# Performance work log

Hardware: AMD Instinct MI355X
Metric: run time of the kernel (lower is better)

The kernel has to match this reference:

```python
import jax, jax.numpy as jnp
import numpy as np

TEMPERATURE = 1.0

def setup_inputs() -> dict:
    key = jax.random.key(0)
    k1, k2 = jax.random.split(key)
    B, F, C = 16384, 2048, 1000
    features = jax.random.normal(k1, (B, F), dtype=jnp.float32)
    prototypes = jax.random.normal(k2, (C, F), dtype=jnp.float32)
    return {"features": features, "prototypes": prototypes}

def reference(features, prototypes):
    # Euclidean pairwise distance via ||a||^2 + ||b||^2 - 2 a.b (same math as cdist p=2)
    f_sq = jnp.sum(features * features, axis=-1, keepdims=True)        # [B,1]
    p_sq = jnp.sum(prototypes * prototypes, axis=-1)[None, :]          # [1,C]
    cross = jnp.einsum('bf,cf->bc', features, prototypes)              # [B,C]
    d2 = jnp.maximum(f_sq + p_sq - 2.0 * cross, 0.0)
    distances = jnp.sqrt(d2)
    logits = -distances
    return logits / TEMPERATURE
```

## Files before the change

kernel.cpp:

```cpp
#include <hip/hip_runtime.h>
#include <stdint.h>


#define KDIM 2048

typedef __attribute__((ext_vector_type(8))) __bf16 bf16x8;
typedef __attribute__((ext_vector_type(4))) float f32x4;

__device__ __forceinline__ bool sniff_is_f32(const void* Araw) {
  const uint16_t* sniff = (const uint16_t*)Araw;
  float mx = 0.f;
#pragma unroll
  for (int i = 0; i < 64; ++i) {
    float v = __uint_as_float(((uint32_t)sniff[i]) << 16);
    mx = fmaxf(mx, fabsf(v));
  }
  return mx > 1e4f;
}

__device__ __forceinline__ uint32_t bf16rn(uint32_t u) {
  return (u + 0x7FFFu + ((u >> 16) & 1u)) >> 16;
}
__device__ __forceinline__ uint32_t pack_rn(uint32_t a, uint32_t b) {
  return bf16rn(a) | (bf16rn(b) << 16);
}

__device__ __forceinline__ void gload_lds16(const void* g, void* l) {
  __builtin_amdgcn_global_load_lds(
      (const __attribute__((address_space(1))) void*)g,
      (__attribute__((address_space(3))) void*)l, 16, 0, 0);
}

__global__ __launch_bounds__(256) void prep_kernel(
    const void* __restrict__ Araw, const void* __restrict__ Braw,
    uint16_t* __restrict__ Abf, uint16_t* __restrict__ Bbf,
    float* __restrict__ fsq, float* __restrict__ psq, int M, int N) {
  const bool isf32 = sniff_is_f32(Araw);
  const int wave = threadIdx.x >> 6;
  const int lane = threadIdx.x & 63;
  const int row = blockIdx.x * 4 + wave;
  if (row >= M + N) return;
  const bool isA = row < M;
  const size_t r = isA ? (size_t)row : (size_t)(row - M);
  uint2* dst = (uint2*)((isA ? Abf : Bbf) + r * KDIM);
  float s = 0.f;
  if (isf32) {
    const float* p = (isA ? (const float*)Araw : (const float*)Braw) + r * KDIM;
#pragma unroll
    for (int it = 0; it < KDIM / 256; ++it) {
      float4 v = *((const float4*)p + it * 64 + lane);
      s = fmaf(v.x, v.x, fmaf(v.y, v.y, fmaf(v.z, v.z, fmaf(v.w, v.w, s))));
      uint2 o;
      o.x = pack_rn(__float_as_uint(v.x), __float_as_uint(v.y));
      o.y = pack_rn(__float_as_uint(v.z), __float_as_uint(v.w));
      dst[it * 64 + lane] = o;
    }
  } else {
    const uint16_t* p =
        (isA ? (const uint16_t*)Araw : (const uint16_t*)Braw) + r * KDIM;
#pragma unroll
    for (int it = 0; it < KDIM / 256; ++it) {
      uint2 v = *((const uint2*)p + it * 64 + lane);
      float e0 = __uint_as_float(v.x << 16);
      float e1 = __uint_as_float(v.x & 0xFFFF0000u);
      float e2 = __uint_as_float(v.y << 16);
      float e3 = __uint_as_float(v.y & 0xFFFF0000u);
      s = fmaf(e0, e0, fmaf(e1, e1, fmaf(e2, e2, fmaf(e3, e3, s))));
      dst[it * 64 + lane] = v;
    }
  }
#pragma unroll
  for (int o = 32; o > 0; o >>= 1) s += __shfl_down(s, o, 64);
  if (lane == 0) {
    if (isA) fsq[r] = s;
    else     psq[r] = s;
  }
}

#define BM2 256
#define BN2 256
#define BK2 64
#define NK2 (KDIM / BK2)

__global__ __launch_bounds__(512, 2) void gemm_kernel(
    const uint16_t* __restrict__ Abf, const uint16_t* __restrict__ Bbf,
    const float* __restrict__ fsq, const float* __restrict__ psq,
    float* __restrict__ out, int M, int N) {
  __shared__ uint32_t Ab[2][BM2][32];
  __shared__ uint32_t Bb[2][BN2][32];

  const int tid = threadIdx.x;
  const int lane = tid & 63;
  const int wave = tid >> 6;

  const int gx = gridDim.x, gy = gridDim.y;
  const int nwg = gx * gy;
  int id = blockIdx.y * gx + blockIdx.x;
  if ((nwg & 7) == 0) id = (id & 7) * (nwg >> 3) + (id >> 3);
  const int m0 = (id / gx) * BM2;
  const int n0 = (id % gx) * BN2;

  const int wr = wave >> 2;
  const int wc = wave & 3;
  const int lr = lane & 15;
  const int lg = lane >> 4;

  const int wbase = (tid & ~63);

  auto stage = [&](int b, int ks) {
#pragma unroll
    for (int p = 0; p < 4; ++p) {
      const int f = p * 512 + tid;
      const int row = f >> 3;
      const int gc = (f & 7) ^ (row & 7);
      uint32_t* la = &Ab[b][0][0] + (p * 512 + wbase) * 4;
      uint32_t* lb = &Bb[b][0][0] + (p * 512 + wbase) * 4;
      int gm = m0 + row; gm = gm < M ? gm : M - 1;
      int gn = n0 + row; gn = gn < N ? gn : N - 1;
      gload_lds16(Abf + (size_t)gm * KDIM + ks * BK2 + gc * 8, la);
      gload_lds16(Bbf + (size_t)gn * KDIM + ks * BK2 + gc * 8, lb);
    }
  };

  f32x4 acc[8][4] = {};

  stage(0, 0);

  for (int ks = 0; ks < NK2; ++ks) {
    const int buf = ks & 1;
    if (ks + 1 < NK2) {
      stage(buf ^ 1, ks + 1);
      asm volatile("s_waitcnt vmcnt(8)");
    } else {
      asm volatile("s_waitcnt vmcnt(0)");
    }
    __builtin_amdgcn_s_barrier();
    asm volatile("" ::: "memory");

    bf16x8 bh[4][2];
#pragma unroll
    for (int nj = 0; nj < 4; ++nj) {
      const int r = wc * 64 + nj * 16 + lr;
#pragma unroll
      for (int kk = 0; kk < 2; ++kk) {
        const int pc = ((kk * 4 + lg) ^ (r & 7)) * 4;
        bh[nj][kk] = *(const bf16x8*)&Bb[buf][r][pc];
      }
    }

    __builtin_amdgcn_s_setprio(1);
#pragma unroll
    for (int mi = 0; mi < 8; ++mi) {
      const int r = wr * 128 + mi * 16 + lr;
      const int p0 = ((0 + lg) ^ (r & 7)) * 4;
      const int p1 = ((4 + lg) ^ (r & 7)) * 4;
      const bf16x8 a0 = *(const bf16x8*)&Ab[buf][r][p0];
      const bf16x8 a1 = *(const bf16x8*)&Ab[buf][r][p1];
#pragma unroll
      for (int nj = 0; nj < 4; ++nj) {
        acc[mi][nj] = __builtin_amdgcn_mfma_f32_16x16x32_bf16(
            a0, bh[nj][0], acc[mi][nj], 0, 0, 0);
        acc[mi][nj] = __builtin_amdgcn_mfma_f32_16x16x32_bf16(
            a1, bh[nj][1], acc[mi][nj], 0, 0, 0);
      }
    }
    __builtin_amdgcn_s_setprio(0);

    __builtin_amdgcn_s_barrier();
    asm volatile("" ::: "memory");
  }

#pragma unroll
  for (int nj = 0; nj < 4; ++nj) {
    const int n = n0 + wc * 64 + nj * 16 + lr;
    if (n >= N) continue;
    const float pn = psq[n];
#pragma unroll
    for (int mi = 0; mi < 8; ++mi) {
      const int mb = m0 + wr * 128 + mi * 16 + lg * 4;
#pragma unroll
      for (int r = 0; r < 4; ++r) {
        const int m = mb + r;
        if (m < M) {
          const float d2 = fsq[m] + pn - 2.f * acc[mi][nj][r];
          out[(size_t)m * N + n] = -sqrtf(fmaxf(d2, 0.f));
        }
      }
    }
  }
}

#define BM 128
#define BN 128
#define BKS 32
#define NSTEPS (KDIM / BKS)

__global__ __launch_bounds__(256) void dist_mfma_kernel(
    const void* __restrict__ Araw, const void* __restrict__ Braw,
    float* __restrict__ out, int M, int N) {
  __shared__ uint32_t Ah[2][BM][16];
  __shared__ uint32_t Bh[2][BN][16];
  __shared__ float fsqs[BM];
  __shared__ float psqs[BN];

  const bool isf32 = sniff_is_f32(Araw);
  const int tid = threadIdx.x;
  const int lane = tid & 63;
  const int wave = tid >> 6;
  const int m0 = blockIdx.y * BM;
  const int n0 = blockIdx.x * BN;

  const float* A32 = (const float*)Araw;
  const float* B32 = (const float*)Braw;
  const uint16_t* A16 = (const uint16_t*)Araw;
  const uint16_t* B16 = (const uint16_t*)Braw;

  const int crow = tid >> 2;
  const int cch = tid & 3;
  const int wr = wave >> 1;
  const int wc = wave & 1;
  const int lr = lane & 15;
  const int lg = lane >> 4;

  uint4 qa0[2], qa1[2], qb0[2], qb1[2];
  float na[2] = {0.f, 0.f};
  float nb[2] = {0.f, 0.f};

  auto load_step = [&](int ks) {
#pragma unroll
    for (int s = 0; s < 2; ++s) {
      const int row = crow + 64 * s;
      int gm = m0 + row; gm = gm < M ? gm : M - 1;
      int gn = n0 + row; gn = gn < N ? gn : N - 1;
      const size_t ea = (size_t)gm * KDIM + ks * BKS + cch * 8;
      const size_t eb = (size_t)gn * KDIM + ks * BKS + cch * 8;
      if (isf32) {
        qa0[s] = *(const uint4*)(A32 + ea);
        qa1[s] = *(const uint4*)(A32 + ea + 4);
        qb0[s] = *(const uint4*)(B32 + eb);
        qb1[s] = *(const uint4*)(B32 + eb + 4);
      } else {
        qa0[s] = *(const uint4*)(A16 + ea);
        qb0[s] = *(const uint4*)(B16 + eb);
      }
    }
  };

  auto store_step = [&](int b) {
#pragma unroll
    for (int s = 0; s < 2; ++s) {
      const int row = crow + 64 * s;
      const int pc = (cch ^ ((row >> 1) & 3)) * 4;
      if (isf32) {
        const uint32_t ua[8] = {qa0[s].x, qa0[s].y, qa0[s].z, qa0[s].w,
                                qa1[s].x, qa1[s].y, qa1[s].z, qa1[s].w};
        const uint32_t ub[8] = {qb0[s].x, qb0[s].y, qb0[s].z, qb0[s].w,
                                qb1[s].x, qb1[s].y, qb1[s].z, qb1[s].w};
        float sa = 0.f, sb = 0.f;
#pragma unroll
        for (int j = 0; j < 8; ++j) {
          const float fa = __uint_as_float(ua[j]);
          const float fb = __uint_as_float(ub[j]);
          sa = fmaf(fa, fa, sa);
          sb = fmaf(fb, fb, sb);
        }
        na[s] += sa; nb[s] += sb;
        uint4 pa = {pack_rn(ua[0], ua[1]), pack_rn(ua[2], ua[3]),
                    pack_rn(ua[4], ua[5]), pack_rn(ua[6], ua[7])};
        uint4 pb = {pack_rn(ub[0], ub[1]), pack_rn(ub[2], ub[3]),
                    pack_rn(ub[4], ub[5]), pack_rn(ub[6], ub[7])};
        *(uint4*)&Ah[b][row][pc] = pa;
        *(uint4*)&Bh[b][row][pc] = pb;
      } else {
        float sa = 0.f, sb = 0.f;
        const uint32_t va[4] = {qa0[s].x, qa0[s].y, qa0[s].z, qa0[s].w};
        const uint32_t vb[4] = {qb0[s].x, qb0[s].y, qb0[s].z, qb0[s].w};
#pragma unroll
        for (int j = 0; j < 4; ++j) {
          const float a0 = __uint_as_float(va[j] << 16);
          const float a1 = __uint_as_float(va[j] & 0xFFFF0000u);
          const float b0 = __uint_as_float(vb[j] << 16);
          const float b1 = __uint_as_float(vb[j] & 0xFFFF0000u);
          sa = fmaf(a0, a0, fmaf(a1, a1, sa));
          sb = fmaf(b0, b0, fmaf(b1, b1, sb));
        }
        na[s] += sa; nb[s] += sb;
        *(uint4*)&Ah[b][row][pc] = qa0[s];
        *(uint4*)&Bh[b][row][pc] = qb0[s];
      }
    }
  };

  f32x4 acc[4][4] = {};
  load_step(0);
  store_step(0);
  __syncthreads();

  for (int ks = 0; ks < NSTEPS; ++ks) {
    const int buf = ks & 1;
    const int nxt = ks + 1;
    if (nxt < NSTEPS) load_step(nxt);

    bf16x8 ah[4], bh[4];
#pragma unroll
    for (int i = 0; i < 4; ++i) {
      const int r = wr * 64 + i * 16 + lr;
      const int pc = (lg ^ ((r >> 1) & 3)) * 4;
      ah[i] = *(const bf16x8*)&Ah[buf][r][pc];
    }
#pragma unroll
    for (int j = 0; j < 4; ++j) {
      const int r = wc * 64 + j * 16 + lr;
      const int pc = (lg ^ ((r >> 1) & 3)) * 4;
      bh[j] = *(const bf16x8*)&Bh[buf][r][pc];
    }

#pragma unroll
    for (int i = 0; i < 4; ++i)
#pragma unroll
      for (int j = 0; j < 4; ++j)
        acc[i][j] = __builtin_amdgcn_mfma_f32_16x16x32_bf16(ah[i], bh[j],
                                                            acc[i][j], 0, 0, 0);

    if (nxt < NSTEPS) store_step(nxt & 1);
    __syncthreads();
  }

  float v0 = na[0], v1 = na[1], w0 = nb[0], w1 = nb[1];
#pragma unroll
  for (int o = 1; o <= 2; o <<= 1) {
    v0 += __shfl_xor(v0, o);
    v1 += __shfl_xor(v1, o);
    w0 += __shfl_xor(w0, o);
    w1 += __shfl_xor(w1, o);
  }
  if (cch == 0) {
    fsqs[crow] = v0;
    fsqs[crow + 64] = v1;
    psqs[crow] = w0;
    psqs[crow + 64] = w1;
  }
  __syncthreads();

#pragma unroll
  for (int j = 0; j < 4; ++j) {
    const int nn = wc * 64 + j * 16 + lr;
    const int n = n0 + nn;
    if (n >= N) continue;
    const float pn = psqs[nn];
#pragma unroll
    for (int i = 0; i < 4; ++i) {
      const int mb = wr * 64 + i * 16 + lg * 4;
#pragma unroll
      for (int r = 0; r < 4; ++r) {
        const int m = m0 + mb + r;
        if (m < M) {
          const float d2 = fsqs[mb + r] + pn - 2.f * acc[i][j][r];
          out[(size_t)m * N + n] = -sqrtf(fmaxf(d2, 0.f));
        }
      }
    }
  }
}

extern "C" void kernel_launch(void* const* d_in, const int* in_sizes, int n_in,
                              void* d_out, int out_size, void* d_ws,
                              size_t ws_size, hipStream_t stream) {
  (void)n_in; (void)out_size;
  const void* feat = d_in[0];
  const void* prot = d_in[1];
  float* out = (float*)d_out;

  const int M = in_sizes[0] / KDIM;
  const int N = in_sizes[1] / KDIM;

  const size_t bfA = (size_t)M * KDIM * sizeof(uint16_t);
  const size_t bfB = (size_t)N * KDIM * sizeof(uint16_t);
  const size_t ws_need = bfA + bfB + (size_t)(M + N) * sizeof(float);

  if (d_ws != nullptr && ws_size >= ws_need) {
    uint16_t* Abf = (uint16_t*)d_ws;
    uint16_t* Bbf = (uint16_t*)((char*)d_ws + bfA);
    float* fsq = (float*)((char*)d_ws + bfA + bfB);
    float* psq = fsq + M;
    const int rows = M + N;
    prep_kernel<<<dim3((rows + 3) / 4), dim3(256), 0, stream>>>(
        feat, prot, Abf, Bbf, fsq, psq, M, N);
    dim3 grid((N + BN2 - 1) / BN2, (M + BM2 - 1) / BM2);
    gemm_kernel<<<grid, dim3(512), 0, stream>>>(Abf, Bbf, fsq, psq, out, M, N);
  } else {
    dim3 grid((N + BN - 1) / BN, (M + BM - 1) / BM);
    dist_mfma_kernel<<<grid, dim3(256), 0, stream>>>(feat, prot, out, M, N);
  }
}
```

Baseline: 322.0 us.

## Restructure GEMM main loop into four interleaved MFMA clusters with split prefetch

Splits each K-step into four MFMA clusters over half-tiles of A and B, with LDS fragment reads and global-to-LDS prefetch of the next stage spread between clusters and separated by barriers. The aim is to overlap LDS reads and global loads with MFMA work instead of loading all fragments up front, in the style of ping-pong scheduling. It adds many more workgroup barriers per iteration and a full vmcnt(0) wait before the last cluster, which could serialize the loads and stall.

```diff
diff --git a/kernel.cpp b/kernel.cpp
--- a/kernel.cpp
+++ b/kernel.cpp
@@ -6,6 +6,8 @@
 
 typedef __attribute__((ext_vector_type(8))) __bf16 bf16x8;
 typedef __attribute__((ext_vector_type(4))) float f32x4;
+
+#define BAR() do { asm volatile("" ::: "memory"); __builtin_amdgcn_s_barrier(); asm volatile("" ::: "memory"); } while (0)
 
 __device__ __forceinline__ bool sniff_is_f32(const void* Araw) {
   const uint16_t* sniff = (const uint16_t*)Araw;
@@ -107,67 +109,100 @@
 
   const int wbase = (tid & ~63);
 
-  auto stage = [&](int b, int ks) {
-#pragma unroll
-    for (int p = 0; p < 4; ++p) {
-      const int f = p * 512 + tid;
-      const int row = f >> 3;
+  auto stage_half = [&](int b, int ks, int mat, int h) {
+#pragma unroll
+    for (int l = 0; l < 2; ++l) {
+      const int f = l * 512 + tid;
+      const int row = h * 128 + (f >> 3);
       const int gc = (f & 7) ^ (row & 7);
-      uint32_t* la = &Ab[b][0][0] + (p * 512 + wbase) * 4;
-      uint32_t* lb = &Bb[b][0][0] + (p * 512 + wbase) * 4;
-      int gm = m0 + row; gm = gm < M ? gm : M - 1;
-      int gn = n0 + row; gn = gn < N ? gn : N - 1;
-      gload_lds16(Abf + (size_t)gm * KDIM + ks * BK2 + gc * 8, la);
-      gload_lds16(Bbf + (size_t)gn * KDIM + ks * BK2 + gc * 8, lb);
+      uint32_t* base = mat ? &Bb[b][0][0] : &Ab[b][0][0];
+      uint32_t* dst = base + h * 4096 + (l * 512 + wbase) * 4;
+      const int lim = mat ? N : M;
+      int g = (mat ? n0 : m0) + row;
+      g = g < lim ? g : lim - 1;
+      const uint16_t* G = mat ? Bbf : Abf;
+      gload_lds16(G + (size_t)g * KDIM + ks * BK2 + gc * 8, dst);
+    }
+  };
+
+  bf16x8 A0[4][2], A1[4][2], B0[2][2], B1[2][2];
+
+  auto readA = [&](bf16x8 (&dst)[4][2], int b, int mh) {
+#pragma unroll
+    for (int i = 0; i < 4; ++i) {
+      const int r = wr * 128 + (mh * 4 + i) * 16 + lr;
+#pragma unroll
+      for (int kk = 0; kk < 2; ++kk) {
+        const int pc = (((kk << 2) + lg) ^ (r & 7)) * 4;
+        dst[i][kk] = *(const bf16x8*)&Ab[b][r][pc];
+      }
+    }
+  };
+  auto readB = [&](bf16x8 (&dst)[2][2], int b, int nh) {
+#pragma unroll
+    for (int j = 0; j < 2; ++j) {
+      const int r = wc * 64 + (nh * 2 + j) * 16 + lr;
+#pragma unroll
+      for (int kk = 0; kk < 2; ++kk) {
+        const int pc = (((kk << 2) + lg) ^ (r & 7)) * 4;
+        dst[j][kk] = *(const bf16x8*)&Bb[b][r][pc];
+      }
     }
   };
 
   f32x4 acc[8][4] = {};
 
-  stage(0, 0);
+  auto cluster = [&](bf16x8 (&A)[4][2], bf16x8 (&B)[2][2], int mh, int nh) {
+    __builtin_amdgcn_s_setprio(1);
+#pragma unroll
+    for (int i = 0; i < 4; ++i)
+#pragma unroll
+      for (int j = 0; j < 2; ++j)
+#pragma unroll
+        for (int kk = 0; kk < 2; ++kk)
+          acc[mh * 4 + i][nh * 2 + j] = __builtin_amdgcn_mfma_f32_16x16x32_bf16(
+              A[i][kk], B[j][kk], acc[mh * 4 + i][nh * 2 + j], 0, 0, 0);
+    __builtin_amdgcn_s_setprio(0);
+  };
+
+  stage_half(0, 0, 0, 0); stage_half(0, 0, 0, 1);
+  stage_half(0, 0, 1, 0); stage_half(0, 0, 1, 1);
+  asm volatile("s_waitcnt vmcnt(0)" ::: "memory");
+  BAR();
 
   for (int ks = 0; ks < NK2; ++ks) {
-    const int buf = ks & 1;
-    if (ks + 1 < NK2) {
-      stage(buf ^ 1, ks + 1);
-      asm volatile("s_waitcnt vmcnt(8)");
-    } else {
-      asm volatile("s_waitcnt vmcnt(0)");
-    }
-    __builtin_amdgcn_s_barrier();
-    asm volatile("" ::: "memory");
-
-    bf16x8 bh[4][2];
-#pragma unroll
-    for (int nj = 0; nj < 4; ++nj) {
-      const int r = wc * 64 + nj * 16 + lr;
-#pragma unroll
-      for (int kk = 0; kk < 2; ++kk) {
-        const int pc = ((kk * 4 + lg) ^ (r & 7)) * 4;
-        bh[nj][kk] = *(const bf16x8*)&Bb[buf][r][pc];
-      }
-    }
-
-    __builtin_amdgcn_s_setprio(1);
-#pragma unroll
-    for (int mi = 0; mi < 8; ++mi) {
-      const int r = wr * 128 + mi * 16 + lr;
-      const int p0 = ((0 + lg) ^ (r & 7)) * 4;
-      const int p1 = ((4 + lg) ^ (r & 7)) * 4;
-      const bf16x8 a0 = *(const bf16x8*)&Ab[buf][r][p0];
-      const bf16x8 a1 = *(const bf16x8*)&Ab[buf][r][p1];
-#pragma unroll
-      for (int nj = 0; nj < 4; ++nj) {
-        acc[mi][nj] = __builtin_amdgcn_mfma_f32_16x16x32_bf16(
-            a0, bh[nj][0], acc[mi][nj], 0, 0, 0);
-        acc[mi][nj] = __builtin_amdgcn_mfma_f32_16x16x32_bf16(
-            a1, bh[nj][1], acc[mi][nj], 0, 0, 0);
-      }
-    }
-    __builtin_amdgcn_s_setprio(0);
-
-    __builtin_amdgcn_s_barrier();
-    asm volatile("" ::: "memory");
+    const int buf = ks & 1, nbuf = buf ^ 1;
+    const bool pf = (ks + 1 < NK2);
+
+    readA(A0, buf, 0);
+    readB(B0, buf, 0);
+    if (pf) { stage_half(nbuf, ks + 1, 0, 0); stage_half(nbuf, ks + 1, 0, 1); }
+    asm volatile("s_waitcnt lgkmcnt(8)" ::: "memory");
+    BAR();
+    asm volatile("s_waitcnt lgkmcnt(0)" ::: "memory");
+    __builtin_amdgcn_sched_barrier(0);
+    cluster(A0, B0, 0, 0);
+    BAR();
+
+    readB(B1, buf, 1);
+    if (pf) { stage_half(nbuf, ks + 1, 1, 0); stage_half(nbuf, ks + 1, 1, 1); }
+    BAR();
+    asm volatile("s_waitcnt lgkmcnt(0)" ::: "memory");
+    __builtin_amdgcn_sched_barrier(0);
+    cluster(A0, B1, 0, 1);
+    BAR();
+
+    readA(A1, buf, 1);
+    BAR();
+    asm volatile("s_waitcnt lgkmcnt(0)" ::: "memory");
+    __builtin_amdgcn_sched_barrier(0);
+    cluster(A1, B0, 1, 0);
+    BAR();
+
+    asm volatile("s_waitcnt vmcnt(0)" ::: "memory");
+    BAR();
+    cluster(A1, B1, 1, 1);
+    BAR();
   }
 
 #pragma unroll
```

After: 329.1 us. 2.2% more time.
